# Kernel optimization log

Hardware: AMD Instinct MI355X
Metric: run time of the kernel (lower is better)

Reference implementation:

```python
import jax, jax.numpy as jnp
from jax import lax
import numpy as np

B = 65536
DIM_OBS = 9
DIM_ACT = 4
H = 192
DN = ('NCHW', 'OIHW', 'NCHW')


def _conv(x, w, stride):
    return lax.conv_general_dilated(x, w, (stride, stride), 'VALID', dimension_numbers=DN)


def setup_inputs() -> dict:
    key = jax.random.key(0)
    ks = jax.random.split(key, 16)
    n = lambda k, shp, s: (jax.random.normal(k, shp, dtype=jnp.float32) * s)
    inp = {
        'x': n(ks[0], (B, 1, 12, 16), 1.0),
        'v': n(ks[1], (B, DIM_OBS), 1.0),
        'hx': n(ks[2], (B, H), 1.0),
        # stem convs (no bias)
        'w1': n(ks[3], (32, 1, 2, 2), 0.5),
        'w2': n(ks[4], (64, 32, 3, 3), 0.06),
        'w3': n(ks[5], (128, 64, 3, 3), 0.04),
        'w_stem': n(ks[6], (H, 128 * 2 * 4), 0.03),   # Linear(1024, 192, bias=False)
        # v_proj (weight scaled by 0.5 as in __init__)
        'w_vproj': n(ks[7], (H, DIM_OBS), 0.5 / np.sqrt(DIM_OBS)),
        'b_vproj': n(ks[8], (H,), 0.1),
        # GRUCell(192, 192): gate order r, z, n
        'w_ih': n(ks[9], (3 * H, H), 1.0 / np.sqrt(H)),
        'w_hh': n(ks[10], (3 * H, H), 1.0 / np.sqrt(H)),
        'b_ih': n(ks[11], (3 * H,), 0.05),
        'b_hh': n(ks[12], (3 * H,), 0.05),
        # fc (weight scaled by 0.01 as in __init__)
        'w_fc': n(ks[13], (DIM_ACT, H), 0.01 / np.sqrt(H)),
    }
    return inp


def reference(x, v, hx, w1, w2, w3, w_stem, w_vproj, b_vproj,
              w_ih, w_hh, b_ih, b_hh, w_fc):
    lrelu = lambda t: jax.nn.leaky_relu(t, 0.05)
    # vision stem: [B,1,12,16] -> [B,32,6,8] -> [B,64,4,6] -> [B,128,2,4]
    h = lrelu(_conv(x, w1, 2))
    h = lrelu(_conv(h, w2, 1))
    h = lrelu(_conv(h, w3, 1))
    img_feat = h.reshape(h.shape[0], -1) @ w_stem.T          # [B,192]
    state_feat = v @ w_vproj.T + b_vproj                      # [B,192]
    fused = lrelu(img_feat + state_feat)
    # GRUCell (torch gate order: r, z, n)
    gi = fused @ w_ih.T + b_ih                                # [B,576]
    gh = hx @ w_hh.T + b_hh                                   # [B,576]
    ir, iz, i_n = jnp.split(gi, 3, axis=-1)
    hr, hz, h_n = jnp.split(gh, 3, axis=-1)
    r = jax.nn.sigmoid(ir + hr)
    z = jax.nn.sigmoid(iz + hz)
    n = jnp.tanh(i_n + r * h_n)
    hx_new = (1.0 - z) * n + z * hx
    act = lrelu(hx_new) @ w_fc.T                              # [B,4]
    return act, hx_new
```

## Files before the change

### kernel.cpp

```cpp
#include <hip/hip_runtime.h>


typedef short bf8 __attribute__((ext_vector_type(8)));
typedef float f4  __attribute__((ext_vector_type(4)));

#define MFMA(a, b, c) __builtin_amdgcn_mfma_f32_16x16x32_bf16(a, b, c, 0, 0, 0)

#define W3_OFF    18432
#define WSTEM_OFF 92160
#define WIH_OFF   294912
#define WHH_OFF   405504
#define W_TOTAL   516096
#define C3_OFF    (1 << 20)
#define C2Q_OFF   68157440

__device__ __forceinline__ unsigned short f2bf(float f) {
    unsigned int u = __float_as_uint(f);
    u += 0x7fffu + ((u >> 16) & 1u);
    return (unsigned short)(u >> 16);
}
__device__ __forceinline__ float bf2f(unsigned short h) {
    return __uint_as_float(((unsigned int)h) << 16);
}
__device__ __forceinline__ float lrelu(float v) { return v > 0.f ? v : 0.05f * v; }
__device__ __forceinline__ float sigm(float x) { return 1.f / (1.f + __expf(-x)); }
__device__ __forceinline__ float tanh_(float x) {
    float e = __expf(2.f * x);
    return 1.f - 2.f / (e + 1.f);
}

__global__ void prep_weights(const float* __restrict__ w2, const float* __restrict__ w3,
                             const float* __restrict__ wstem, const float* __restrict__ wvp,
                             const float* __restrict__ wih, const float* __restrict__ whh,
                             unsigned short* __restrict__ o) {
    int i = blockIdx.x * 256 + threadIdx.x;
    if (i >= W_TOTAL) return;
    float val;
    if (i < W3_OFF) {
        int n = i / 288, k = i - n * 288;
        val = w2[n * 288 + (k & 31) * 9 + (k >> 5)];
    } else if (i < WSTEM_OFF) {
        int d = i - W3_OFF;
        int n = d / 576, k = d - n * 576;
        val = w3[n * 576 + (k & 63) * 9 + (k >> 6)];
    } else if (i < WIH_OFF) {
        int d = i - WSTEM_OFF;
        int n = d / 1056, k = d - n * 1056;
        if (k < 1024)       val = wstem[(n << 10) + (k & 127) * 8 + (k >> 7)];
        else if (k < 1033)  val = wvp[n * 9 + (k - 1024)];
        else                val = 0.f;
    } else if (i < WHH_OFF) {
        val = wih[i - WIH_OFF];
    } else {
        val = whh[i - WHH_OFF];
    }
    o[i] = f2bf(val);
}

__global__ __launch_bounds__(256, 2) void conv12(
    const float* __restrict__ x, const float* __restrict__ w1,
    const unsigned short* __restrict__ ws, unsigned short* __restrict__ c2q,
    int sbase)
{
    __shared__ __align__(16) unsigned short lds[6144];
    const int tid = threadIdx.x;
    const int wave = tid >> 6, lane = tid & 63;
    const int col = lane & 15, quad = lane >> 4;
    const int W0 = blockIdx.x * 32;

    bf8 Bf2[9];
    int kq2[9];
    #pragma unroll
    for (int ks = 0; ks < 9; ++ks) {
        int k0 = ks * 32 + quad * 8;
        Bf2[ks] = *(const bf8*)(ws + (wave * 16 + col) * 288 + k0);
        int ky = k0 / 96, r = k0 - 96 * ky;
        kq2[ks] = (ky * 8 + (r >> 5)) * 32 + (r & 31);
    }
    const int g = wave * 2 + (col >> 3);

    for (int c = 0; c < 8; ++c) {
        if (tid < 192) {
            int s = tid / 48, p = tid - s * 48;
            int y = p >> 3, xx = p & 7;
            const float* xp = x + (size_t)(sbase + W0 + c * 4 + s) * 192 + y * 32 + xx * 2;
            float x00 = xp[0], x01 = xp[1], x10 = xp[16], x11 = xp[17];
            int base = s * 1536, sw = (s & 3) << 3;
            #pragma unroll
            for (int cc = 0; cc < 32; ++cc) {
                int co = (cc + p) & 31;
                float a = x00 * w1[co * 4] + x01 * w1[co * 4 + 1]
                        + x10 * w1[co * 4 + 2] + x11 * w1[co * 4 + 3];
                lds[base + ((p * 32 + co) ^ sw)] = f2bf(lrelu(a));
            }
        }
        __syncthreads();

        #pragma unroll
        for (int mt2 = 0; mt2 < 3; ++mt2) {
            int m0 = mt2 * 32 + col, m1 = m0 + 16;
            int s0 = m0 & 3, p0 = m0 >> 2;
            int s1 = m1 & 3, p1 = m1 >> 2;
            int oy0 = p0 / 6, ox0 = p0 - 6 * oy0;
            int oy1 = p1 / 6, ox1 = p1 - 6 * oy1;
            int b0 = s0 * 1536, qb0 = (oy0 * 8 + ox0) * 32, sw0 = (s0 & 3) << 3;
            int b1 = s1 * 1536, qb1 = (oy1 * 8 + ox1) * 32, sw1 = (s1 & 3) << 3;
            f4 acc0 = {0.f, 0.f, 0.f, 0.f}, acc1 = {0.f, 0.f, 0.f, 0.f};
            #pragma unroll
            for (int ks = 0; ks < 9; ++ks) {
                bf8 a0 = *(const bf8*)&lds[b0 + ((qb0 + kq2[ks]) ^ sw0)];
                bf8 a1 = *(const bf8*)&lds[b1 + ((qb1 + kq2[ks]) ^ sw1)];
                acc0 = MFMA(a0, Bf2[ks], acc0);
                acc1 = MFMA(a1, Bf2[ks], acc1);
            }
            #pragma unroll
            for (int r = 0; r < 4; ++r) {
                int m = mt2 * 32 + quad * 4 + r;
                int s = m & 3, pos = m >> 2;
                int sloc = W0 + c * 4 + s;
                int key = (pos + ((sloc & 1) << 2)) & 7;
                c2q[(size_t)sloc * 1536 + pos * 64 + ((g ^ key) << 3) + (col & 7)]
                    = f2bf(lrelu(acc0[r]));
                m += 16; s = m & 3; pos = m >> 2;
                sloc = W0 + c * 4 + s;
                key = (pos + ((sloc & 1) << 2)) & 7;
                c2q[(size_t)sloc * 1536 + pos * 64 + ((g ^ key) << 3) + (col & 7)]
                    = f2bf(lrelu(acc1[r]));
            }
        }
        __syncthreads();
    }
}

__global__ __launch_bounds__(256, 2) void conv3k(
    const unsigned short* __restrict__ ws, const unsigned short* __restrict__ c2q,
    unsigned short* __restrict__ c3, int sbase)
{
    __shared__ __align__(16) unsigned short lds[12288];
    const int tid = threadIdx.x;
    const int wave = tid >> 6, lane = tid & 63;
    const int col = lane & 15, quad = lane >> 4;
    const int h = blockIdx.x & 1;
    const int Q0 = (blockIdx.x >> 1) * 64;
    const int n_in = h * 64 + wave * 16 + col;

    bf8 Bf3[18];
    #pragma unroll
    for (int ks = 0; ks < 18; ++ks)
        Bf3[ks] = *(const bf8*)(ws + W3_OFF + n_in * 576 + ks * 32 + quad * 8);

    int aoff[18];
    {
        int opos = col & 7;
        int oy = opos >> 2, ox = opos & 3;
        int spar = (col >> 3) & 1;
        #pragma unroll
        for (int ks = 0; ks < 18; ++ks) {
            int k0 = ks * 32 + quad * 8;
            int b = k0 >> 6;
            int ky = b / 3, kx = b - 3 * ky;
            int pos2 = (oy + ky) * 6 + (ox + kx);
            int gg = (k0 & 63) >> 3;
            int key = (pos2 + (spar << 2)) & 7;
            aoff[ks] = pos2 * 64 + ((gg ^ key) << 3);
        }
    }
    const int Gl = h * 8 + wave * 2 + (col >> 3);

    for (int c = 0; c < 8; ++c) {
        const unsigned short* s2 = c2q + (size_t)(Q0 + c * 8) * 1536 + tid * 48;
        #pragma unroll
        for (int i = 0; i < 6; ++i)
            *(bf8*)&lds[tid * 48 + i * 8] = *(const bf8*)(s2 + i * 8);
        __syncthreads();

        f4 acc[4];
        #pragma unroll
        for (int mt = 0; mt < 4; ++mt) acc[mt] = (f4){0.f, 0.f, 0.f, 0.f};
        #pragma unroll
        for (int ks = 0; ks < 18; ++ks) {
            #pragma unroll
            for (int mt = 0; mt < 4; ++mt) {
                int sc = mt * 2 + (col >> 3);
                bf8 a = *(const bf8*)&lds[sc * 1536 + aoff[ks]];
                acc[mt] = MFMA(a, Bf3[ks], acc[mt]);
            }
        }
        #pragma unroll
        for (int mt = 0; mt < 4; ++mt) {
            #pragma unroll
            for (int r = 0; r < 4; ++r) {
                int m = quad * 4 + r;
                int sc = mt * 2 + (m >> 3), opos = m & 7;
                int srow = sbase + Q0 + c * 8 + sc;
                c3[(size_t)srow * 1024 + opos * 128 + ((Gl ^ (srow & 15)) << 3) + (col & 7)]
                    = f2bf(lrelu(acc[mt][r]));
            }
        }
        __syncthreads();
    }
}

__global__ __launch_bounds__(256, 2) void stem_gru(
    const unsigned short* __restrict__ ws, const float* __restrict__ v,
    const float* __restrict__ hx, const float* __restrict__ bvp,
    const float* __restrict__ bih, const float* __restrict__ bhh,
    const float* __restrict__ wfc, float* __restrict__ out)
{
    __shared__ __align__(16) unsigned short lds[28672];
    const int tid = threadIdx.x;
    const int wave = tid >> 6, lane = tid & 63;
    const int col = lane & 15, quad = lane >> 4;
    const int S0 = blockIdx.x * 64;
    const unsigned short* c3 = ws + C3_OFF;
    const unsigned short* wstem = ws + WSTEM_OFF;

    f4 acc[4][3];
    #pragma unroll
    for (int mt = 0; mt < 4; ++mt)
        #pragma unroll
        for (int t = 0; t < 3; ++t) acc[mt][t] = (f4){0.f, 0.f, 0.f, 0.f};

    const int sm = tid >> 2, sq = tid & 3;
    const unsigned short* asrc = c3 + (size_t)(S0 + sm) * 1024 + sq * 32;

    #pragma unroll
    for (int i = 0; i < 4; ++i)
        *(bf8*)&lds[12288 + sm * 128 + sq * 32 + i * 8] = *(const bf8*)(asrc + i * 8);
    __syncthreads();

    for (int kc = 0; kc < 8; ++kc) {
        bf8 nx[4];
        if (kc < 7) {
            const unsigned short* s2 = asrc + (kc + 1) * 128;
            #pragma unroll
            for (int i = 0; i < 4; ++i) nx[i] = *(const bf8*)(s2 + i * 8);
        }
        int abase = 12288 + (kc & 1) * 8192;
        #pragma unroll
        for (int ks = 0; ks < 4; ++ks) {
            int kl = ks * 32 + quad * 8;
            int kk = kc * 128 + kl;
            bf8 b0 = *(const bf8*)(wstem + (wave * 48 + col) * 1056 + kk);
            bf8 b1 = *(const bf8*)(wstem + (wave * 48 + 16 + col) * 1056 + kk);
            bf8 b2 = *(const bf8*)(wstem + (wave * 48 + 32 + col) * 1056 + kk);
            #pragma unroll
            for (int mt = 0; mt < 4; ++mt) {
                int m = mt * 16 + col;
                bf8 a = *(const bf8*)&lds[abase + m * 128 + (kl ^ ((m & 15) << 3))];
                acc[mt][0] = MFMA(a, b0, acc[mt][0]);
                acc[mt][1] = MFMA(a, b1, acc[mt][1]);
                acc[mt][2] = MFMA(a, b2, acc[mt][2]);
            }
        }
        if (kc < 7) {
            int wb = 12288 + ((kc + 1) & 1) * 8192;
            #pragma unroll
            for (int i = 0; i < 4; ++i)
                *(bf8*)&lds[wb + sm * 128 + sq * 32 + i * 8] = nx[i];
        }
        __syncthreads();
    }

    if (tid < 64) {
        int m = tid;
        const float* vp = v + (size_t)(S0 + m) * 9;
        __align__(16) unsigned short tmp[32];
        #pragma unroll
        for (int i = 0; i < 9; ++i) tmp[i] = f2bf(vp[i]);
        #pragma unroll
        for (int i = 9; i < 32; ++i) tmp[i] = 0;
        #pragma unroll
        for (int gg = 0; gg < 4; ++gg) {
            int gp = gg ^ (m & 15);
            *(bf8*)&lds[12288 + m * 128 + gp * 8] = *(bf8*)&tmp[gg * 8];
        }
    }
    __syncthreads();
    {
        int kl = quad * 8;
        bf8 b0 = *(const bf8*)(wstem + (wave * 48 + col) * 1056 + 1024 + kl);
        bf8 b1 = *(const bf8*)(wstem + (wave * 48 + 16 + col) * 1056 + 1024 + kl);
        bf8 b2 = *(const bf8*)(wstem + (wave * 48 + 32 + col) * 1056 + 1024 + kl);
        #pragma unroll
        for (int mt = 0; mt < 4; ++mt) {
            int m = mt * 16 + col;
            bf8 a = *(const bf8*)&lds[12288 + m * 128 + (kl ^ ((m & 15) << 3))];
            acc[mt][0] = MFMA(a, b0, acc[mt][0]);
            acc[mt][1] = MFMA(a, b1, acc[mt][1]);
            acc[mt][2] = MFMA(a, b2, acc[mt][2]);
        }
    }

    #pragma unroll
    for (int t = 0; t < 3; ++t) {
        int n = wave * 48 + t * 16 + col;
        float bb = bvp[n];
        #pragma unroll
        for (int mt = 0; mt < 4; ++mt)
            #pragma unroll
            for (int r = 0; r < 4; ++r) {
                int m = mt * 16 + quad * 4 + r;
                lds[m * 192 + (n ^ ((m & 7) << 3))] = f2bf(lrelu(acc[mt][t][r] + bb));
            }
    }
    __syncthreads();

    {
        int m = tid >> 2, qq = tid & 3;
        const float* hp = hx + (size_t)(S0 + m) * 192 + qq * 48;
        #pragma unroll
        for (int i = 0; i < 6; ++i) {
            f4 d = *(const f4*)(hp + i * 8 + 0);
            f4 d2 = *(const f4*)(hp + i * 8 + 4);
            __align__(16) unsigned short tmp[8];
            #pragma unroll
            for (int u = 0; u < 4; ++u) { tmp[u] = f2bf(d[u]); tmp[4 + u] = f2bf(d2[u]); }
            int gg = qq * 6 + i, gp = gg ^ (m & 7);
            *(bf8*)&lds[12288 + m * 192 + gp * 8] = *(bf8*)tmp;
        }
    }
    __syncthreads();

    #pragma unroll
    for (int t = 0; t < 3; ++t) {
        int j0 = (wave * 3 + t) * 16;
        int j = j0 + col;
        const unsigned short* pih = ws + WIH_OFF + j * 192;
        const unsigned short* phh = ws + WHH_OFF + j * 192;
        f4 g0[4], g1[4], g2[4], g3[4], g4[4], g5[4];
        #pragma unroll
        for (int mt = 0; mt < 4; ++mt) {
            g0[mt] = (f4){0.f,0.f,0.f,0.f}; g1[mt] = g0[mt]; g2[mt] = g0[mt];
            g3[mt] = g0[mt]; g4[mt] = g0[mt]; g5[mt] = g0[mt];
        }
        #pragma unroll
        for (int ks = 0; ks < 6; ++ks) {
            int k0 = ks * 32 + quad * 8;
            bf8 bir = *(const bf8*)(pih + k0);
            bf8 bhr = *(const bf8*)(phh + k0);
            bf8 biz = *(const bf8*)(pih + 36864 + k0);
            bf8 bhz = *(const bf8*)(phh + 36864 + k0);
            bf8 bin = *(const bf8*)(pih + 73728 + k0);
            bf8 bhn = *(const bf8*)(phh + 73728 + k0);
            #pragma unroll
            for (int mt = 0; mt < 4; ++mt) {
                int m = mt * 16 + col;
                int off = m * 192 + (k0 ^ ((m & 7) << 3));
                bf8 aF = *(const bf8*)&lds[off];
                bf8 aH = *(const bf8*)&lds[12288 + off];
                g0[mt] = MFMA(aF, bir, g0[mt]);
                g1[mt] = MFMA(aH, bhr, g1[mt]);
                g2[mt] = MFMA(aF, biz, g2[mt]);
                g3[mt] = MFMA(aH, bhz, g3[mt]);
                g4[mt] = MFMA(aF, bin, g4[mt]);
                g5[mt] = MFMA(aH, bhn, g5[mt]);
            }
        }
        float b_ir = bih[j], b_iz = bih[192 + j], b_in = bih[384 + j];
        float b_hr = bhh[j], b_hz = bhh[192 + j], b_hn = bhh[384 + j];
        #pragma unroll
        for (int mt = 0; mt < 4; ++mt)
            #pragma unroll
            for (int r = 0; r < 4; ++r) {
                int s = mt * 16 + quad * 4 + r;
                float rg = sigm(g0[mt][r] + b_ir + g1[mt][r] + b_hr);
                float zg = sigm(g2[mt][r] + b_iz + g3[mt][r] + b_hz);
                float ng = tanh_(g4[mt][r] + b_in + rg * (g5[mt][r] + b_hn));
                float hxv = hx[(size_t)(S0 + s) * 192 + j];
                float hnew = (1.f - zg) * ng + zg * hxv;
                out[65536 * 4 + (size_t)(S0 + s) * 192 + j] = hnew;
            }
    }
    __syncthreads();

    {
        int s = tid & 63, a = tid >> 6;
        const float* hp = out + 65536 * 4 + (size_t)(S0 + s) * 192;
        const float* wf = wfc + a * 192;
        float sum = 0.f;
        #pragma unroll 4
        for (int jj = 0; jj < 48; ++jj) {
            f4 hv = *(const f4*)(hp + jj * 4);
            f4 wv = *(const f4*)(wf + jj * 4);
            #pragma unroll
            for (int u = 0; u < 4; ++u) sum += lrelu(hv[u]) * wv[u];
        }
        out[(size_t)(S0 + s) * 4 + a] = sum;
    }
}

extern "C" void kernel_launch(void* const* d_in, const int* in_sizes, int n_in,
                              void* d_out, int out_size, void* d_ws, size_t ws_size,
                              hipStream_t stream) {
    const float* x     = (const float*)d_in[0];
    const float* v     = (const float*)d_in[1];
    const float* hx    = (const float*)d_in[2];
    const float* w1    = (const float*)d_in[3];
    const float* w2    = (const float*)d_in[4];
    const float* w3    = (const float*)d_in[5];
    const float* wstem = (const float*)d_in[6];
    const float* wvp   = (const float*)d_in[7];
    const float* bvp   = (const float*)d_in[8];
    const float* wih   = (const float*)d_in[9];
    const float* whh   = (const float*)d_in[10];
    const float* bih   = (const float*)d_in[11];
    const float* bhh   = (const float*)d_in[12];
    const float* wfc   = (const float*)d_in[13];
    unsigned short* wsp = (unsigned short*)d_ws;
    unsigned short* c3  = wsp + C3_OFF;
    unsigned short* c2q = wsp + C2Q_OFF;

    prep_weights<<<2016, 256, 0, stream>>>(w2, w3, wstem, wvp, wih, whh, wsp);
    for (int q = 0; q < 4; ++q) {
        conv12<<<512, 256, 0, stream>>>(x, w1, wsp, c2q, q * 16384);
        conv3k<<<512, 256, 0, stream>>>(wsp, c2q, c3, q * 16384);
    }
    stem_gru<<<1024, 256, 0, stream>>>(wsp, v, hx, bvp, bih, bhh, wfc, (float*)d_out);
}
```

Before: 581.6 us.

## Raise occupancy: smaller conv blocks, single-buffer stem LDS, split GRU rows

The conv kernels now process half as many samples per block and launch twice as many blocks, with higher launch-bound occupancy targets. The stem/GRU kernel drops its LDS double buffer for a single buffer with extra barriers, and processes the hx tile in two 32-row halves to shrink LDS to about 40 KB and cut accumulator registers. The aim is more resident waves per CU to hide memory latency. The cost is more synchronisation, lost load/compute overlap in the stem loop, and repeated weight loads across the two GRU halves.

```diff
diff --git a/kernel.cpp b/kernel.cpp
--- a/kernel.cpp
+++ b/kernel.cpp
@@ -13,6 +13,7 @@
 #define W_TOTAL   516096
 #define C3_OFF    (1 << 20)
 #define C2Q_OFF   68157440
+#define SCR       12288
 
 __device__ __forceinline__ unsigned short f2bf(float f) {
     unsigned int u = __float_as_uint(f);
@@ -57,7 +58,7 @@
     o[i] = f2bf(val);
 }
 
-__global__ __launch_bounds__(256, 2) void conv12(
+__global__ __launch_bounds__(256, 4) void conv12(
     const float* __restrict__ x, const float* __restrict__ w1,
     const unsigned short* __restrict__ ws, unsigned short* __restrict__ c2q,
     int sbase)
@@ -66,7 +67,7 @@
     const int tid = threadIdx.x;
     const int wave = tid >> 6, lane = tid & 63;
     const int col = lane & 15, quad = lane >> 4;
-    const int W0 = blockIdx.x * 32;
+    const int W0 = blockIdx.x * 16;
 
     bf8 Bf2[9];
     int kq2[9];
@@ -79,7 +80,7 @@
     }
     const int g = wave * 2 + (col >> 3);
 
-    for (int c = 0; c < 8; ++c) {
+    for (int c = 0; c < 4; ++c) {
         if (tid < 192) {
             int s = tid / 48, p = tid - s * 48;
             int y = p >> 3, xx = p & 7;
@@ -132,7 +133,7 @@
     }
 }
 
-__global__ __launch_bounds__(256, 2) void conv3k(
+__global__ __launch_bounds__(256, 3) void conv3k(
     const unsigned short* __restrict__ ws, const unsigned short* __restrict__ c2q,
     unsigned short* __restrict__ c3, int sbase)
 {
@@ -141,7 +142,7 @@
     const int wave = tid >> 6, lane = tid & 63;
     const int col = lane & 15, quad = lane >> 4;
     const int h = blockIdx.x & 1;
-    const int Q0 = (blockIdx.x >> 1) * 64;
+    const int Q0 = (blockIdx.x >> 1) * 32;
     const int n_in = h * 64 + wave * 16 + col;
 
     bf8 Bf3[18];
@@ -167,7 +168,7 @@
     }
     const int Gl = h * 8 + wave * 2 + (col >> 3);
 
-    for (int c = 0; c < 8; ++c) {
+    for (int c = 0; c < 4; ++c) {
         const unsigned short* s2 = c2q + (size_t)(Q0 + c * 8) * 1536 + tid * 48;
         #pragma unroll
         for (int i = 0; i < 6; ++i)
@@ -201,13 +202,13 @@
     }
 }
 
-__global__ __launch_bounds__(256, 2) void stem_gru(
+__global__ __launch_bounds__(256, 4) void stem_gru(
     const unsigned short* __restrict__ ws, const float* __restrict__ v,
     const float* __restrict__ hx, const float* __restrict__ bvp,
     const float* __restrict__ bih, const float* __restrict__ bhh,
     const float* __restrict__ wfc, float* __restrict__ out)
 {
-    __shared__ __align__(16) unsigned short lds[28672];
+    __shared__ __align__(16) unsigned short lds[20480];
     const int tid = threadIdx.x;
     const int wave = tid >> 6, lane = tid & 63;
     const int col = lane & 15, quad = lane >> 4;
@@ -226,17 +227,16 @@
 
     #pragma unroll
     for (int i = 0; i < 4; ++i)
-        *(bf8*)&lds[12288 + sm * 128 + sq * 32 + i * 8] = *(const bf8*)(asrc + i * 8);
-    __syncthreads();
+        *(bf8*)&lds[SCR + sm * 128 + sq * 32 + i * 8] = *(const bf8*)(asrc + i * 8);
 
     for (int kc = 0; kc < 8; ++kc) {
+        __syncthreads();
         bf8 nx[4];
         if (kc < 7) {
             const unsigned short* s2 = asrc + (kc + 1) * 128;
             #pragma unroll
             for (int i = 0; i < 4; ++i) nx[i] = *(const bf8*)(s2 + i * 8);
         }
-        int abase = 12288 + (kc & 1) * 8192;
         #pragma unroll
         for (int ks = 0; ks < 4; ++ks) {
             int kl = ks * 32 + quad * 8;
@@ -247,19 +247,18 @@
             #pragma unroll
             for (int mt = 0; mt < 4; ++mt) {
                 int m = mt * 16 + col;
-                bf8 a = *(const bf8*)&lds[abase + m * 128 + (kl ^ ((m & 15) << 3))];
+                bf8 a = *(const bf8*)&lds[SCR + m * 128 + (kl ^ ((m & 15) << 3))];
                 acc[mt][0] = MFMA(a, b0, acc[mt][0]);
                 acc[mt][1] = MFMA(a, b1, acc[mt][1]);
                 acc[mt][2] = MFMA(a, b2, acc[mt][2]);
             }
         }
+        __syncthreads();
         if (kc < 7) {
-            int wb = 12288 + ((kc + 1) & 1) * 8192;
             #pragma unroll
             for (int i = 0; i < 4; ++i)
-                *(bf8*)&lds[wb + sm * 128 + sq * 32 + i * 8] = nx[i];
-        }
-        __syncthreads();
+                *(bf8*)&lds[SCR + sm * 128 + sq * 32 + i * 8] = nx[i];
+        }
     }
 
     if (tid < 64) {
@@ -273,7 +272,7 @@
         #pragma unroll
         for (int gg = 0; gg < 4; ++gg) {
             int gp = gg ^ (m & 15);
-            *(bf8*)&lds[12288 + m * 128 + gp * 8] = *(bf8*)&tmp[gg * 8];
+            *(bf8*)&lds[SCR + m * 128 + gp * 8] = *(bf8*)&tmp[gg * 8];
         }
     }
     __syncthreads();
@@ -285,7 +284,7 @@
         #pragma unroll
         for (int mt = 0; mt < 4; ++mt) {
             int m = mt * 16 + col;
-            bf8 a = *(const bf8*)&lds[12288 + m * 128 + (kl ^ ((m & 15) << 3))];
+            bf8 a = *(const bf8*)&lds[SCR + m * 128 + (kl ^ ((m & 15) << 3))];
             acc[mt][0] = MFMA(a, b0, acc[mt][0]);
             acc[mt][1] = MFMA(a, b1, acc[mt][1]);
             acc[mt][2] = MFMA(a, b2, acc[mt][2]);
@@ -306,71 +305,76 @@
     }
     __syncthreads();
 
-    {
-        int m = tid >> 2, qq = tid & 3;
-        const float* hp = hx + (size_t)(S0 + m) * 192 + qq * 48;
-        #pragma unroll
-        for (int i = 0; i < 6; ++i) {
-            f4 d = *(const f4*)(hp + i * 8 + 0);
-            f4 d2 = *(const f4*)(hp + i * 8 + 4);
-            __align__(16) unsigned short tmp[8];
-            #pragma unroll
-            for (int u = 0; u < 4; ++u) { tmp[u] = f2bf(d[u]); tmp[4 + u] = f2bf(d2[u]); }
-            int gg = qq * 6 + i, gp = gg ^ (m & 7);
-            *(bf8*)&lds[12288 + m * 192 + gp * 8] = *(bf8*)tmp;
-        }
-    }
-    __syncthreads();
-
-    #pragma unroll
-    for (int t = 0; t < 3; ++t) {
-        int j0 = (wave * 3 + t) * 16;
-        int j = j0 + col;
-        const unsigned short* pih = ws + WIH_OFF + j * 192;
-        const unsigned short* phh = ws + WHH_OFF + j * 192;
-        f4 g0[4], g1[4], g2[4], g3[4], g4[4], g5[4];
-        #pragma unroll
-        for (int mt = 0; mt < 4; ++mt) {
-            g0[mt] = (f4){0.f,0.f,0.f,0.f}; g1[mt] = g0[mt]; g2[mt] = g0[mt];
-            g3[mt] = g0[mt]; g4[mt] = g0[mt]; g5[mt] = g0[mt];
-        }
-        #pragma unroll
-        for (int ks = 0; ks < 6; ++ks) {
-            int k0 = ks * 32 + quad * 8;
-            bf8 bir = *(const bf8*)(pih + k0);
-            bf8 bhr = *(const bf8*)(phh + k0);
-            bf8 biz = *(const bf8*)(pih + 36864 + k0);
-            bf8 bhz = *(const bf8*)(phh + 36864 + k0);
-            bf8 bin = *(const bf8*)(pih + 73728 + k0);
-            bf8 bhn = *(const bf8*)(phh + 73728 + k0);
-            #pragma unroll
-            for (int mt = 0; mt < 4; ++mt) {
-                int m = mt * 16 + col;
-                int off = m * 192 + (k0 ^ ((m & 7) << 3));
-                bf8 aF = *(const bf8*)&lds[off];
-                bf8 aH = *(const bf8*)&lds[12288 + off];
-                g0[mt] = MFMA(aF, bir, g0[mt]);
-                g1[mt] = MFMA(aH, bhr, g1[mt]);
-                g2[mt] = MFMA(aF, biz, g2[mt]);
-                g3[mt] = MFMA(aH, bhz, g3[mt]);
-                g4[mt] = MFMA(aF, bin, g4[mt]);
-                g5[mt] = MFMA(aH, bhn, g5[mt]);
-            }
-        }
-        float b_ir = bih[j], b_iz = bih[192 + j], b_in = bih[384 + j];
-        float b_hr = bhh[j], b_hz = bhh[192 + j], b_hn = bhh[384 + j];
-        #pragma unroll
-        for (int mt = 0; mt < 4; ++mt)
-            #pragma unroll
-            for (int r = 0; r < 4; ++r) {
-                int s = mt * 16 + quad * 4 + r;
-                float rg = sigm(g0[mt][r] + b_ir + g1[mt][r] + b_hr);
-                float zg = sigm(g2[mt][r] + b_iz + g3[mt][r] + b_hz);
-                float ng = tanh_(g4[mt][r] + b_in + rg * (g5[mt][r] + b_hn));
-                float hxv = hx[(size_t)(S0 + s) * 192 + j];
-                float hnew = (1.f - zg) * ng + zg * hxv;
-                out[65536 * 4 + (size_t)(S0 + s) * 192 + j] = hnew;
-            }
+    for (int p = 0; p < 2; ++p) {
+        if (p) __syncthreads();
+        if (tid < 128) {
+            int m = tid >> 2, qq = tid & 3;
+            const float* hp = hx + (size_t)(S0 + p * 32 + m) * 192 + qq * 48;
+            #pragma unroll
+            for (int i = 0; i < 6; ++i) {
+                f4 d = *(const f4*)(hp + i * 8 + 0);
+                f4 d2 = *(const f4*)(hp + i * 8 + 4);
+                __align__(16) unsigned short tmp[8];
+                #pragma unroll
+                for (int u = 0; u < 4; ++u) { tmp[u] = f2bf(d[u]); tmp[4 + u] = f2bf(d2[u]); }
+                int gg = qq * 6 + i, gp = gg ^ (m & 7);
+                *(bf8*)&lds[SCR + m * 192 + gp * 8] = *(bf8*)tmp;
+            }
+        }
+        __syncthreads();
+
+        #pragma unroll
+        for (int t = 0; t < 3; ++t) {
+            int j0 = (wave * 3 + t) * 16;
+            int j = j0 + col;
+            const unsigned short* pih = ws + WIH_OFF + j * 192;
+            const unsigned short* phh = ws + WHH_OFF + j * 192;
+            f4 g0[2], g1[2], g2[2], g3[2], g4[2], g5[2];
+            #pragma unroll
+            for (int mt = 0; mt < 2; ++mt) {
+                g0[mt] = (f4){0.f,0.f,0.f,0.f}; g1[mt] = g0[mt]; g2[mt] = g0[mt];
+                g3[mt] = g0[mt]; g4[mt] = g0[mt]; g5[mt] = g0[mt];
+            }
+            #pragma unroll
+            for (int ks = 0; ks < 6; ++ks) {
+                int k0 = ks * 32 + quad * 8;
+                bf8 bir = *(const bf8*)(pih + k0);
+                bf8 bhr = *(const bf8*)(phh + k0);
+                bf8 biz = *(const bf8*)(pih + 36864 + k0);
+                bf8 bhz = *(const bf8*)(phh + 36864 + k0);
+                bf8 bin = *(const bf8*)(pih + 73728 + k0);
+                bf8 bhn = *(const bf8*)(phh + 73728 + k0);
+                #pragma unroll
+                for (int mt = 0; mt < 2; ++mt) {
+                    int ml = mt * 16 + col;
+                    int mg = p * 32 + ml;
+                    int offF = mg * 192 + (k0 ^ ((mg & 7) << 3));
+                    int offH = ml * 192 + (k0 ^ ((ml & 7) << 3));
+                    bf8 aF = *(const bf8*)&lds[offF];
+                    bf8 aH = *(const bf8*)&lds[SCR + offH];
+                    g0[mt] = MFMA(aF, bir, g0[mt]);
+                    g1[mt] = MFMA(aH, bhr, g1[mt]);
+                    g2[mt] = MFMA(aF, biz, g2[mt]);
+                    g3[mt] = MFMA(aH, bhz, g3[mt]);
+                    g4[mt] = MFMA(aF, bin, g4[mt]);
+                    g5[mt] = MFMA(aH, bhn, g5[mt]);
+                }
+            }
+            float b_ir = bih[j], b_iz = bih[192 + j], b_in = bih[384 + j];
+            float b_hr = bhh[j], b_hz = bhh[192 + j], b_hn = bhh[384 + j];
+            #pragma unroll
+            for (int mt = 0; mt < 2; ++mt)
+                #pragma unroll
+                for (int r = 0; r < 4; ++r) {
+                    int s = p * 32 + mt * 16 + quad * 4 + r;
+                    float rg = sigm(g0[mt][r] + b_ir + g1[mt][r] + b_hr);
+                    float zg = sigm(g2[mt][r] + b_iz + g3[mt][r] + b_hz);
+                    float ng = tanh_(g4[mt][r] + b_in + rg * (g5[mt][r] + b_hn));
+                    float hxv = hx[(size_t)(S0 + s) * 192 + j];
+                    float hnew = (1.f - zg) * ng + zg * hxv;
+                    out[65536 * 4 + (size_t)(S0 + s) * 192 + j] = hnew;
+                }
+        }
     }
     __syncthreads();
 
@@ -413,8 +417,8 @@
 
     prep_weights<<<2016, 256, 0, stream>>>(w2, w3, wstem, wvp, wih, whh, wsp);
     for (int q = 0; q < 4; ++q) {
-        conv12<<<512, 256, 0, stream>>>(x, w1, wsp, c2q, q * 16384);
-        conv3k<<<512, 256, 0, stream>>>(wsp, c2q, c3, q * 16384);
+        conv12<<<1024, 256, 0, stream>>>(x, w1, wsp, c2q, q * 16384);
+        conv3k<<<1024, 256, 0, stream>>>(wsp, c2q, c3, q * 16384);
     }
     stem_gru<<<1024, 256, 0, stream>>>(wsp, v, hx, bvp, bih, bhh, wfc, (float*)d_out);
 }
```

Result: slower. 1.402 ms (+141.0%).
